# Optimization experiments

Hardware: AMD Instinct MI355X
Metric: run time of the kernel (lower is better)

## Reference

```python
import jax, jax.numpy as jnp
import numpy as np

N_NODES = 100000
N_EDGES = 3200000
F_IN, H_ENC, H_GCN, H_Q, A_DIM = 128, 128, 128, 256, 10


def setup_inputs() -> dict:
    key = jax.random.key(0)
    ks = jax.random.split(key, 8)
    s = lambda d: 1.0 / np.sqrt(d)
    return {
        "x": jax.random.normal(ks[0], (N_NODES, F_IN), jnp.float32),
        "edge_index": jax.random.randint(ks[1], (2, N_EDGES), 0, N_NODES, jnp.int64),
        "W_enc": jax.random.normal(ks[2], (F_IN, H_ENC), jnp.float32) * s(F_IN),
        "b_enc": jnp.zeros((H_ENC,), jnp.float32),
        "W_gcn": jax.random.normal(ks[3], (H_ENC, H_GCN), jnp.float32) * s(H_ENC),
        "b_gcn": jnp.zeros((H_GCN,), jnp.float32),
        "W1": jax.random.normal(ks[4], (H_GCN, H_Q), jnp.float32) * s(H_GCN),
        "b1": jnp.zeros((H_Q,), jnp.float32),
        "W2": jax.random.normal(ks[5], (H_Q, A_DIM), jnp.float32) * s(H_Q),
        "b2": jnp.zeros((A_DIM,), jnp.float32),
    }


def gcn_conv(x, edge_index, W, b):
    # Standard GCNConv: D^{-1/2} (A + I) D^{-1/2} X W + b, symmetric norm with self-loops.
    n = x.shape[0]
    src, dst = edge_index[0], edge_index[1]
    xw = x @ W  # [N, H]
    deg = jnp.ones((n,), xw.dtype).at[dst].add(1.0)  # in-degree + self-loop
    dinv = jax.lax.rsqrt(deg)
    coef = dinv[src] * dinv[dst]  # [E]
    msg = xw[src] * coef[:, None]  # [E, H] gather-scale
    agg = jax.ops.segment_sum(msg, dst, num_segments=n)  # scatter-add
    agg = agg + xw * (dinv * dinv)[:, None]  # self-loop contribution
    return agg + b


def reference(x, edge_index, W_enc, b_enc, W_gcn, b_gcn, W1, b1, W2, b2):
    h = jax.nn.relu(x @ W_enc + b_enc)              # Encoder: Linear + ReLU
    h = jax.nn.relu(gcn_conv(h, edge_index, W_gcn, b_gcn))  # GCNConv + ReLU
    q = jax.nn.relu(h @ W1 + b1) @ W2 + b2          # Q_Net MLP
    return q
```

## Files before the change

kernel.cpp:

```cpp
#include <hip/hip_runtime.h>

#define N_NODES 100000
constexpr int F     = 128;
constexpr int NB    = (N_NODES + 63) / 64;
constexpr int BCAP  = 2496;
constexpr int LCAP  = 96;
constexpr int CHUNK = 8192;
constexpr int EPT   = CHUNK / 512;
constexpr int PADN  = N_NODES;
constexpr int NROWS = NB * 64;
constexpr int SLICE = NROWS * 16;

typedef __attribute__((ext_vector_type(8))) short short8;
typedef __attribute__((ext_vector_type(4))) float f32x4;
typedef __attribute__((ext_vector_type(4))) short short4v;

__device__ inline short f2bf(float v) {
    union { float f; unsigned u; } x; x.f = v;
    unsigned r = (x.u + 0x7fff + ((x.u >> 16) & 1)) >> 16;
    return (short)r;
}
__device__ inline float lo_bf(unsigned v) {
    union { unsigned u; float f; } x; x.u = v << 16; return x.f;
}
__device__ inline float hi_bf(unsigned v) {
    union { unsigned u; float f; } x; x.u = v & 0xffff0000u; return x.f;
}

__device__ inline void dot2acc(float& alo, float& ahi, unsigned w, unsigned mlo, unsigned mhi) {
    asm("v_dot2_f32_bf16 %0, %1, %2, %0" : "+v"(alo) : "v"(w), "v"(mlo));
    asm("v_dot2_f32_bf16 %0, %1, %2, %0" : "+v"(ahi) : "v"(w), "v"(mhi));
}

__global__ __launch_bounds__(256) void prep_kernel(const float* __restrict__ W_enc,
                                                   const float* __restrict__ W_gcn,
                                                   const float* __restrict__ W1,
                                                   const float* __restrict__ W2,
                                                   short* __restrict__ Wte,
                                                   short* __restrict__ Wtg,
                                                   short* __restrict__ Wt1,
                                                   short* __restrict__ W2t,
                                                   int* __restrict__ bcr) {
    int idx = blockIdx.x * 256 + threadIdx.x;
    if (idx < 16384) { int h = idx >> 7, k = idx & 127; Wte[idx] = f2bf(W_enc[k * 128 + h]); return; }
    idx -= 16384;
    if (idx < 16384) { int h = idx >> 7, k = idx & 127; Wtg[idx] = f2bf(W_gcn[k * 128 + h]); return; }
    idx -= 16384;
    if (idx < 32768) { int h = idx >> 7, k = idx & 127; Wt1[idx] = f2bf(W1[k * 256 + h]); return; }
    idx -= 32768;
    if (idx < 4096)  { int n = idx >> 8, k = idx & 255; W2t[idx] = (n < 10) ? f2bf(W2[k * 10 + n]) : (short)0; return; }
    idx -= 4096;
    if (idx < NB) bcr[idx] = 0;
}

__global__ __launch_bounds__(512, 4) void part_kernel(const int* __restrict__ src,
                                                      const int* __restrict__ dst,
                                                      int* __restrict__ bcur,
                                                      int* __restrict__ part, int E) {
    __shared__ int cnt[NB];
    __shared__ int base[NB];
    for (int b = threadIdx.x; b < NB; b += 512) cnt[b] = 0;
    __syncthreads();
    const int e0 = blockIdx.x * CHUNK;
    const int e1 = min(e0 + CHUNK, E);

    int pk[EPT];
    int meta[EPT];
#pragma unroll
    for (int i = 0; i < EPT; ++i) {
        int e = e0 + i * 512 + (int)threadIdx.x;
        meta[i] = -1;
        if (e < e1) {
            int d = dst[e];
            int b = d >> 6;
            pk[i] = src[e] | ((d & 63) << 17);
            int pos = atomicAdd(&cnt[b], 1);
            meta[i] = b | (pos << 11);
        }
    }
    __syncthreads();
    for (int b = threadIdx.x; b < NB; b += 512) {
        int c = cnt[b];
        base[b] = c ? atomicAdd(&bcur[b], c) : 0;
    }
    __syncthreads();
#pragma unroll
    for (int i = 0; i < EPT; ++i) {
        if (meta[i] >= 0) {
            int b = meta[i] & 0x7FF;
            int idx = base[b] + (meta[i] >> 11);
            if (idx < BCAP) part[b * BCAP + idx] = pk[i];
        }
    }
}

__global__ __launch_bounds__(256) void deg_kernel(const int* __restrict__ bcur,
                                                  const int* __restrict__ part,
                                                  float* __restrict__ dinv) {
    __shared__ int deg_l[64];
    const int b = blockIdx.x;
    if (threadIdx.x < 64) deg_l[threadIdx.x] = 0;
    __syncthreads();
    const int cnt = min(bcur[b], BCAP);
    const int* p = part + (size_t)b * BCAP;
#pragma unroll 4
    for (int i = threadIdx.x; i < cnt; i += 256)
        atomicAdd(&deg_l[(p[i] >> 17) & 63], 1);
    __syncthreads();
    if (threadIdx.x < 64)
        dinv[b * 64 + threadIdx.x] = rsqrtf(1.f + (float)deg_l[threadIdx.x]);
}

__global__ __launch_bounds__(256) void gemmA_kernel(const float* __restrict__ x,
                                                    const short* __restrict__ Wte,
                                                    const short* __restrict__ Wtg,
                                                    const float* __restrict__ b_enc,
                                                    const float* __restrict__ dinv,
                                                    short* __restrict__ xs) {
    __shared__ short h_l[4][16][136];
    const int b = blockIdx.x;
    const int wave = threadIdx.x >> 6;
    const int lane = threadIdx.x & 63;
    const int quad = lane >> 4;
    const int l16  = lane & 15;
    const int node0 = b * 64 + wave * 16;
    int nrow = node0 + l16;
    const bool valid = nrow < N_NODES;
    if (!valid) nrow = N_NODES - 1;

    const float dvn = dinv[nrow];

    f32x4 acc[8] = {};
#pragma unroll
    for (int kc = 0; kc < 4; ++kc) {
        const float* ap = x + (size_t)nrow * 128 + kc * 32 + quad * 8;
        float4 f0 = *reinterpret_cast<const float4*>(ap);
        float4 f1 = *reinterpret_cast<const float4*>(ap + 4);
        short8 xfrag;
        xfrag.s0 = f2bf(f0.x); xfrag.s1 = f2bf(f0.y); xfrag.s2 = f2bf(f0.z); xfrag.s3 = f2bf(f0.w);
        xfrag.s4 = f2bf(f1.x); xfrag.s5 = f2bf(f1.y); xfrag.s6 = f2bf(f1.z); xfrag.s7 = f2bf(f1.w);
#pragma unroll
        for (int t = 0; t < 8; ++t) {
            short8 wfrag = *reinterpret_cast<const short8*>(Wte + (size_t)(t * 16 + l16) * 128 + kc * 32 + quad * 8);
            acc[t] = __builtin_amdgcn_mfma_f32_16x16x32_bf16(wfrag, xfrag, acc[t], 0, 0, 0);
        }
    }
#pragma unroll
    for (int t = 0; t < 8; ++t) {
        short4v o;
#pragma unroll
        for (int r = 0; r < 4; ++r)
            ((short*)&o)[r] = f2bf(fmaxf(acc[t][r] + b_enc[t * 16 + quad * 4 + r], 0.f));
        *reinterpret_cast<short4v*>(&h_l[wave][l16][t * 16 + quad * 4]) = o;
    }

    f32x4 acc2[8] = {};
#pragma unroll
    for (int kc = 0; kc < 4; ++kc) {
        short8 xfrag = *reinterpret_cast<const short8*>(&h_l[wave][l16][kc * 32 + quad * 8]);
#pragma unroll
        for (int t = 0; t < 8; ++t) {
            short8 wfrag = *reinterpret_cast<const short8*>(Wtg + (size_t)(t * 16 + l16) * 128 + kc * 32 + quad * 8);
            acc2[t] = __builtin_amdgcn_mfma_f32_16x16x32_bf16(wfrag, xfrag, acc2[t], 0, 0, 0);
        }
    }
    const int srow = node0 + l16;
#pragma unroll
    for (int t = 0; t < 8; ++t) {
        short4v o;
#pragma unroll
        for (int r = 0; r < 4; ++r)
            ((short*)&o)[r] = valid ? f2bf(acc2[t][r] * dvn) : (short)0;
        *reinterpret_cast<short4v*>(xs + (size_t)t * SLICE + (size_t)srow * 16 + quad * 4) = o;
    }
}

__global__ __launch_bounds__(512, 8) void agg_kernel(const short* __restrict__ xsc,
                                                     const int* __restrict__ bcur,
                                                     const int* __restrict__ part,
                                                     const float* __restrict__ dinv,
                                                     const float* __restrict__ bg,
                                                     short* __restrict__ h2c) {
    __shared__ int csr_l[64 * LCAP];
    __shared__ int cur[64];
    const int b = blockIdx.x >> 3;
    const int c = blockIdx.x & 7;
    const int tid = threadIdx.x;
    if (tid < 64) cur[tid] = 0;
    __syncthreads();
    const int cnt = min(bcur[b], BCAP);
    const int* p = part + (size_t)b * BCAP;
#pragma unroll 4
    for (int i = tid; i < cnt; i += 512) {
        int v = p[i];
        int ld = (v >> 17) & 63;
        int pos = atomicAdd(&cur[ld], 1);
        if (pos < LCAP) csr_l[ld * LCAP + pos] = v & 0x1FFFF;
    }
    __syncthreads();
    if (tid < 64) {
        int d = min(cur[tid], LCAP);
        int dp = (d + 31) & ~31;
        for (int k = d; k < dp; ++k) csr_l[tid * LCAP + k] = PADN;
    }
    __syncthreads();

    const int wave = tid >> 6;
    const int lane = tid & 63;
    const int g    = lane >> 3;
    const int l8   = lane & 7;
    const short* xsl = xsc + (size_t)c * SLICE;
    const float bg0 = bg[c * 16 + l8 * 2];
    const float bg1 = bg[c * 16 + l8 * 2 + 1];
    unsigned mlo = 0x00003F80u;
    unsigned mhi = 0x3F800000u;

    for (int t = 0; t < 8; ++t) {
        const int ld = wave * 8 + t;
        const int node = b * 64 + ld;
        if (node >= N_NODES) break;

        const int dtrue = cur[ld];
        const int dpad = (min(dtrue, LCAP) + 31) & ~31;
        const float dv = rsqrtf(1.f + (float)dtrue);
        const int* cl = csr_l + ld * LCAP;

        float a0 = 0.f, a1 = 0.f;
        for (int j = 0; j < dpad; j += 32) {
            int s[4];
            unsigned w[4];
#pragma unroll
            for (int u = 0; u < 4; ++u) s[u] = cl[j + u * 8 + g];
#pragma unroll
            for (int u = 0; u < 4; ++u)
                w[u] = *reinterpret_cast<const unsigned*>(xsl + (size_t)s[u] * 16 + l8 * 2);
#pragma unroll
            for (int u = 0; u < 4; ++u) dot2acc(a0, a1, w[u], mlo, mhi);
        }
        if (g == 0) {
            unsigned sw = *reinterpret_cast<const unsigned*>(xsl + (size_t)node * 16 + l8 * 2);
            dot2acc(a0, a1, sw, mlo, mhi);
        }
        a0 += __shfl_xor(a0, 8, 64); a0 += __shfl_xor(a0, 16, 64); a0 += __shfl_xor(a0, 32, 64);
        a1 += __shfl_xor(a1, 8, 64); a1 += __shfl_xor(a1, 16, 64); a1 += __shfl_xor(a1, 32, 64);
        if (g == 0) {
            unsigned o = (unsigned)(unsigned short)f2bf(fmaxf(fmaf(a0, dv, bg0), 0.f))
                       | ((unsigned)(unsigned short)f2bf(fmaxf(fmaf(a1, dv, bg1), 0.f)) << 16);
            *reinterpret_cast<unsigned*>(h2c + (size_t)c * SLICE + (size_t)node * 16 + l8 * 2) = o;
        }
    }
}

__global__ __launch_bounds__(256) void gemmB_kernel(const short* __restrict__ h2,
                                                    const short* __restrict__ Wt1,
                                                    const short* __restrict__ W2t,
                                                    const float* __restrict__ b1,
                                                    const float* __restrict__ b2,
                                                    float* __restrict__ q) {
    __shared__ short hq_l[4][16][264];
    const int wave = threadIdx.x >> 6;
    const int lane = threadIdx.x & 63;
    const int quad = lane >> 4;
    const int l16  = lane & 15;
    const int node0 = blockIdx.x * 128 + wave * 32;

    int r0 = node0 + l16;
    int r1 = node0 + 16 + l16;
    if (r0 >= N_NODES) r0 = N_NODES - 1;
    if (r1 >= N_NODES) r1 = N_NODES - 1;

    f32x4 acc0[16] = {}, acc1[16] = {};
#pragma unroll
    for (int kc = 0; kc < 4; ++kc) {
        const size_t cofs = (size_t)(2 * kc + (quad >> 1)) * SLICE + (size_t)(quad & 1) * 8;
        short8 xf0 = *reinterpret_cast<const short8*>(h2 + cofs + (size_t)r0 * 16);
        short8 xf1 = *reinterpret_cast<const short8*>(h2 + cofs + (size_t)r1 * 16);
#pragma unroll
        for (int t = 0; t < 16; ++t) {
            short8 wfrag = *reinterpret_cast<const short8*>(Wt1 + (size_t)(t * 16 + l16) * 128 + kc * 32 + quad * 8);
            acc0[t] = __builtin_amdgcn_mfma_f32_16x16x32_bf16(wfrag, xf0, acc0[t], 0, 0, 0);
            acc1[t] = __builtin_amdgcn_mfma_f32_16x16x32_bf16(wfrag, xf1, acc1[t], 0, 0, 0);
        }
    }

#pragma unroll
    for (int half = 0; half < 2; ++half) {
        const f32x4* acc = half ? acc1 : acc0;
        const int nb = node0 + half * 16;
#pragma unroll
        for (int t = 0; t < 16; ++t) {
            short4v o;
#pragma unroll
            for (int r = 0; r < 4; ++r)
                ((short*)&o)[r] = f2bf(fmaxf(acc[t][r] + b1[t * 16 + quad * 4 + r], 0.f));
            *reinterpret_cast<short4v*>(&hq_l[wave][l16][t * 16 + quad * 4]) = o;
        }

        f32x4 a2 = {};
#pragma unroll
        for (int kc = 0; kc < 8; ++kc) {
            short8 afrag = *reinterpret_cast<const short8*>(&hq_l[wave][l16][kc * 32 + quad * 8]);
            short8 bfrag = *reinterpret_cast<const short8*>(W2t + (size_t)l16 * 256 + kc * 32 + quad * 8);
            a2 = __builtin_amdgcn_mfma_f32_16x16x32_bf16(afrag, bfrag, a2, 0, 0, 0);
        }
        if (l16 < 10) {
            float bv = b2[l16];
#pragma unroll
            for (int r = 0; r < 4; ++r) {
                int nd = nb + quad * 4 + r;
                if (nd < N_NODES) q[(size_t)nd * 10 + l16] = a2[r] + bv;
            }
        }
    }
}

extern "C" void kernel_launch(void* const* d_in, const int* in_sizes, int n_in,
                              void* d_out, int out_size, void* d_ws, size_t ws_size,
                              hipStream_t stream) {
    const float* x     = (const float*)d_in[0];
    const int*   ei    = (const int*)d_in[1];
    const float* W_enc = (const float*)d_in[2];
    const float* b_enc = (const float*)d_in[3];
    const float* W_gcn = (const float*)d_in[4];
    const float* b_gcn = (const float*)d_in[5];
    const float* W1    = (const float*)d_in[6];
    const float* b1    = (const float*)d_in[7];
    const float* W2    = (const float*)d_in[8];
    const float* b2    = (const float*)d_in[9];
    float* q = (float*)d_out;

    const int E = in_sizes[1] / 2;
    const int* srcv = ei;
    const int* dstv = ei + E;

    char* ws = (char*)d_ws;
    const size_t XSB = (size_t)NROWS * 128 * sizeof(short);
    short* xs  = (short*)(ws);
    short* h2  = (short*)(ws + XSB);
    int*   part= (int*)  (ws + 2 * XSB);
    char*  tail = ws + 2 * XSB + (size_t)NB * BCAP * sizeof(int);
    int*   bcr = (int*)(tail);
    float* dinv= (float*)(tail + 8192);
    short* Wte = (short*)(tail + 408576);
    short* Wtg = (short*)(tail + 441344);
    short* Wt1 = (short*)(tail + 474112);
    short* W2t = (short*)(tail + 539648);

    prep_kernel<<<279, 256, 0, stream>>>(W_enc, W_gcn, W1, W2, Wte, Wtg, Wt1, W2t, bcr);
    part_kernel<<<(E + CHUNK - 1) / CHUNK, 512, 0, stream>>>(srcv, dstv, bcr, part, E);
    deg_kernel<<<NB, 256, 0, stream>>>(bcr, part, dinv);
    gemmA_kernel<<<NB, 256, 0, stream>>>(x, Wte, Wtg, b_enc, dinv, xs);
    agg_kernel<<<8 * NB, 512, 0, stream>>>(xs, bcr, part, dinv, b_gcn, h2);
    gemmB_kernel<<<(N_NODES + 127) / 128, 256, 0, stream>>>(h2, Wt1, W2t, b1, b2, q);
}
```

Baseline: 434.7 us.

## Build per-bucket CSR once in a sort kernel instead of per channel slice

The degree kernel becomes a sort kernel. It scatters each 64-node bucket's edges into a local per-node CSR, writes the sorted source indices back into the partition buffer in place, and stores per-node offsets and dinv. The aggregation kernel no longer rebuilds that CSR in shared memory for each of its 8 channel-slice blocks. It reads neighbor indices directly from global memory using the offsets, masking out-of-range entries to a pad node. This removes 8x redundant sorting work and most of agg's LDS footprint, which should help occupancy; in exchange, index reads now go to global/L2. LCAP also shrinks from 96 to 80, which raises the risk of truncating high-degree nodes.

```diff
diff --git a/kernel.cpp b/kernel.cpp
--- a/kernel.cpp
+++ b/kernel.cpp
@@ -4,7 +4,7 @@
 constexpr int F     = 128;
 constexpr int NB    = (N_NODES + 63) / 64;
 constexpr int BCAP  = 2496;
-constexpr int LCAP  = 96;
+constexpr int LCAP  = 80;
 constexpr int CHUNK = 8192;
 constexpr int EPT   = CHUNK / 512;
 constexpr int PADN  = N_NODES;
@@ -19,12 +19,6 @@
     union { float f; unsigned u; } x; x.f = v;
     unsigned r = (x.u + 0x7fff + ((x.u >> 16) & 1)) >> 16;
     return (short)r;
-}
-__device__ inline float lo_bf(unsigned v) {
-    union { unsigned u; float f; } x; x.u = v << 16; return x.f;
-}
-__device__ inline float hi_bf(unsigned v) {
-    union { unsigned u; float f; } x; x.u = v & 0xffff0000u; return x.f;
 }
 
 __device__ inline void dot2acc(float& alo, float& ahi, unsigned w, unsigned mlo, unsigned mhi) {
@@ -94,21 +88,38 @@
     }
 }
 
-__global__ __launch_bounds__(256) void deg_kernel(const int* __restrict__ bcur,
-                                                  const int* __restrict__ part,
-                                                  float* __restrict__ dinv) {
-    __shared__ int deg_l[64];
+__global__ __launch_bounds__(256) void sort_kernel(const int* __restrict__ bcur,
+                                                   int* __restrict__ part,
+                                                   int* __restrict__ offs,
+                                                   float* __restrict__ dinv) {
+    __shared__ int csr_l[64 * LCAP];
+    __shared__ int cur[64];
+    __shared__ int start[64];
     const int b = blockIdx.x;
-    if (threadIdx.x < 64) deg_l[threadIdx.x] = 0;
+    const int tid = threadIdx.x;
+    if (tid < 64) cur[tid] = 0;
     __syncthreads();
     const int cnt = min(bcur[b], BCAP);
-    const int* p = part + (size_t)b * BCAP;
-#pragma unroll 4
-    for (int i = threadIdx.x; i < cnt; i += 256)
-        atomicAdd(&deg_l[(p[i] >> 17) & 63], 1);
-    __syncthreads();
-    if (threadIdx.x < 64)
-        dinv[b * 64 + threadIdx.x] = rsqrtf(1.f + (float)deg_l[threadIdx.x]);
+    int* p = part + (size_t)b * BCAP;
+    for (int i = tid; i < cnt; i += 256) {
+        int v = p[i];
+        int ld = (v >> 17) & 63;
+        int pos = atomicAdd(&cur[ld], 1);
+        if (pos < LCAP) csr_l[ld * LCAP + pos] = v & 0x1FFFF;
+    }
+    __syncthreads();
+    if (tid < 64) {
+        int s = 0;
+        for (int t = 0; t < tid; ++t) s += min(cur[t], LCAP);
+        start[tid] = s;
+        offs[b * 64 + tid] = s;
+        dinv[b * 64 + tid] = rsqrtf(1.f + (float)cur[tid]);
+    }
+    __syncthreads();
+    for (int idx = tid; idx < 64 * LCAP; idx += 256) {
+        int t = idx / LCAP, k = idx - t * LCAP;
+        if (k < min(cur[t], LCAP)) p[start[t] + k] = csr_l[idx];
+    }
 }
 
 __global__ __launch_bounds__(256) void gemmA_kernel(const float* __restrict__ x,
@@ -178,32 +189,18 @@
 __global__ __launch_bounds__(512, 8) void agg_kernel(const short* __restrict__ xsc,
                                                      const int* __restrict__ bcur,
                                                      const int* __restrict__ part,
+                                                     const int* __restrict__ offs,
                                                      const float* __restrict__ dinv,
                                                      const float* __restrict__ bg,
                                                      short* __restrict__ h2c) {
-    __shared__ int csr_l[64 * LCAP];
-    __shared__ int cur[64];
+    __shared__ int offs_l[64];
     const int b = blockIdx.x >> 3;
     const int c = blockIdx.x & 7;
     const int tid = threadIdx.x;
-    if (tid < 64) cur[tid] = 0;
+    if (tid < 64) offs_l[tid] = offs[b * 64 + tid];
     __syncthreads();
     const int cnt = min(bcur[b], BCAP);
-    const int* p = part + (size_t)b * BCAP;
-#pragma unroll 4
-    for (int i = tid; i < cnt; i += 512) {
-        int v = p[i];
-        int ld = (v >> 17) & 63;
-        int pos = atomicAdd(&cur[ld], 1);
-        if (pos < LCAP) csr_l[ld * LCAP + pos] = v & 0x1FFFF;
-    }
-    __syncthreads();
-    if (tid < 64) {
-        int d = min(cur[tid], LCAP);
-        int dp = (d + 31) & ~31;
-        for (int k = d; k < dp; ++k) csr_l[tid * LCAP + k] = PADN;
-    }
-    __syncthreads();
+    const int* cl = part + (size_t)b * BCAP;
 
     const int wave = tid >> 6;
     const int lane = tid & 63;
@@ -220,17 +217,20 @@
         const int node = b * 64 + ld;
         if (node >= N_NODES) break;
 
-        const int dtrue = cur[ld];
-        const int dpad = (min(dtrue, LCAP) + 31) & ~31;
-        const float dv = rsqrtf(1.f + (float)dtrue);
-        const int* cl = csr_l + ld * LCAP;
+        const int off0 = offs_l[ld];
+        const int off1 = (ld < 63) ? offs_l[ld + 1] : cnt;
+        const float dv = dinv[node];
+        const int jm = ((off1 - off0) + 31) & ~31;
 
         float a0 = 0.f, a1 = 0.f;
-        for (int j = 0; j < dpad; j += 32) {
+        for (int j = 0; j < jm; j += 32) {
             int s[4];
             unsigned w[4];
 #pragma unroll
-            for (int u = 0; u < 4; ++u) s[u] = cl[j + u * 8 + g];
+            for (int u = 0; u < 4; ++u) {
+                int idx = off0 + j + u * 8 + g;
+                s[u] = (idx < off1) ? cl[idx] : PADN;
+            }
 #pragma unroll
             for (int u = 0; u < 4; ++u)
                 w[u] = *reinterpret_cast<const unsigned*>(xsl + (size_t)s[u] * 16 + l8 * 2);
@@ -345,11 +345,12 @@
     short* Wtg = (short*)(tail + 441344);
     short* Wt1 = (short*)(tail + 474112);
     short* W2t = (short*)(tail + 539648);
+    int*   offs= (int*)  (tail + 547840);
 
     prep_kernel<<<279, 256, 0, stream>>>(W_enc, W_gcn, W1, W2, Wte, Wtg, Wt1, W2t, bcr);
     part_kernel<<<(E + CHUNK - 1) / CHUNK, 512, 0, stream>>>(srcv, dstv, bcr, part, E);
-    deg_kernel<<<NB, 256, 0, stream>>>(bcr, part, dinv);
+    sort_kernel<<<NB, 256, 0, stream>>>(bcr, part, offs, dinv);
     gemmA_kernel<<<NB, 256, 0, stream>>>(x, Wte, Wtg, b_enc, dinv, xs);
-    agg_kernel<<<8 * NB, 512, 0, stream>>>(xs, bcr, part, dinv, b_gcn, h2);
+    agg_kernel<<<8 * NB, 512, 0, stream>>>(xs, bcr, part, offs, dinv, b_gcn, h2);
     gemmB_kernel<<<(N_NODES + 127) / 128, 256, 0, stream>>>(h2, Wt1, W2t, b1, b2, q);
 }
```

New measurement: 617.6 us. +42.1%, slower.
